# Performance work log

Measured on AMD Instinct MI355X. Metric: run time of the kernel, lower is better.

## Reference

```python
import jax, jax.numpy as jnp
import numpy as np

ALPHA = 1.0

def setup_inputs() -> dict:
    key = jax.random.key(0)
    X = jax.random.normal(key, (8192, 64), dtype=jnp.float32)
    return {"X": X}

def reference(X) -> jnp.ndarray:
    # Pairwise squared L2 distances via GEMM trick: ||x_i||^2 + ||x_j||^2 - 2 x_i.x_j
    sq = jnp.sum(X * X, axis=1)                      # [N]
    d2 = sq[:, None] + sq[None, :] - 2.0 * (X @ X.T)  # [N, N]
    d2 = jnp.maximum(d2, 0.0)
    # sigma^2 = alpha * mean(d2), detached (no grad through bandwidth)
    sigma_sq = ALPHA * jax.lax.stop_gradient(jnp.mean(d2))
    return jnp.exp(-d2 / (2.0 * sigma_sq))
```

## Files before the change

### kernel.cpp

```cpp
#include <hip/hip_runtime.h>
#include <hip/hip_bf16.h>

#define N 8192
#define D 64

typedef __attribute__((ext_vector_type(8))) short bf16x8;
typedef __attribute__((ext_vector_type(4))) float f32x4;

__device__ inline unsigned short f2b(float f) {
    __hip_bfloat16 h = __float2bfloat16(f);
    return __builtin_bit_cast(unsigned short, h);
}

__global__ __launch_bounds__(256) void gk_prep(const float4* __restrict__ X4,
                                               ushort4* __restrict__ Xb4,
                                               float* __restrict__ sq) {
    const int g = blockIdx.x * 256 + threadIdx.x;
    float4 v = X4[g];
    ushort4 b;
    b.x = f2b(v.x); b.y = f2b(v.y); b.z = f2b(v.z); b.w = f2b(v.w);
    Xb4[g] = b;
    float ss = v.x * v.x + v.y * v.y + v.z * v.z + v.w * v.w;
    ss += __shfl_xor(ss, 8, 16);
    ss += __shfl_xor(ss, 4, 16);
    ss += __shfl_xor(ss, 2, 16);
    ss += __shfl_xor(ss, 1, 16);
    if ((threadIdx.x & 15) == 0) sq[g >> 4] = ss;
}

__global__ __launch_bounds__(256) void gk_colsum(const float* __restrict__ X,
                                                 float* __restrict__ V) {
    __shared__ float red[256];
    const int c = blockIdx.x;
    float s = 0.f;
    for (int r = threadIdx.x; r < N; r += 256) s += X[r * D + c];
    red[threadIdx.x] = s;
    __syncthreads();
    for (int off = 128; off > 0; off >>= 1) {
        if (threadIdx.x < off) red[threadIdx.x] += red[threadIdx.x + off];
        __syncthreads();
    }
    if (threadIdx.x == 0) V[c] = red[0];
}

__global__ __launch_bounds__(256) void gk_finalize(const float* __restrict__ sq,
                                                   const float* __restrict__ V,
                                                   float* __restrict__ scal) {
    __shared__ float red[256];
    float s = 0.f;
    for (int r = threadIdx.x; r < N; r += 256) s += sq[r];
    red[threadIdx.x] = s;
    __syncthreads();
    for (int off = 128; off > 0; off >>= 1) {
        if (threadIdx.x < off) red[threadIdx.x] += red[threadIdx.x + off];
        __syncthreads();
    }
    const float S = red[0];
    __syncthreads();
    float v = (threadIdx.x < D) ? V[threadIdx.x] : 0.f;
    red[threadIdx.x] = v * v;
    __syncthreads();
    for (int off = 128; off > 0; off >>= 1) {
        if (threadIdx.x < off) red[threadIdx.x] += red[threadIdx.x + off];
        __syncthreads();
    }
    if (threadIdx.x == 0) {
        const float Vsq = red[0];
        const float fN = (float)N;
        const float mean = 2.f * S / fN - 2.f * Vsq / (fN * fN);
        const float sigma_sq = 1.0f * mean;
        scal[0] = 1.f / (2.f * sigma_sq);
    }
}

__global__ __launch_bounds__(256) void gk_main(const unsigned short* __restrict__ Xb,
                                               const float* __restrict__ sq,
                                               const float* __restrict__ scal,
                                               float* __restrict__ out) {
    const int lane = threadIdx.x & 63;
    const int wave = threadIdx.x >> 6;
    const int i0 = blockIdx.x * 64 + wave * 16;
    const int j0 = blockIdx.y * 128;
    const int m = lane & 15;
    const int q = lane >> 4;
    const float c0 = scal[0];

    const bf16x8* Arow = reinterpret_cast<const bf16x8*>(Xb + (i0 + m) * D + 8 * q);
    const bf16x8 a0 = Arow[0];
    const bf16x8 a1 = Arow[4];

    f32x4 acc[8];
#pragma unroll
    for (int t = 0; t < 8; ++t) acc[t] = (f32x4){0.f, 0.f, 0.f, 0.f};

#pragma unroll
    for (int t = 0; t < 8; ++t) {
        const bf16x8* Brow =
            reinterpret_cast<const bf16x8*>(Xb + (j0 + t * 16 + m) * D + 8 * q);
        const bf16x8 b0 = Brow[0];
        const bf16x8 b1 = Brow[4];
        acc[t] = __builtin_amdgcn_mfma_f32_16x16x32_bf16(a0, b0, acc[t], 0, 0, 0);
        acc[t] = __builtin_amdgcn_mfma_f32_16x16x32_bf16(a1, b1, acc[t], 0, 0, 0);
    }

    float sqi[4];
#pragma unroll
    for (int r = 0; r < 4; ++r) sqi[r] = sq[i0 + 4 * q + r];

#pragma unroll
    for (int t = 0; t < 8; ++t) {
        const int col = j0 + t * 16 + m;
        const float sqj = sq[col];
#pragma unroll
        for (int r = 0; r < 4; ++r) {
            float d2 = sqi[r] + sqj - 2.0f * acc[t][r];
            d2 = fmaxf(d2, 0.0f);
            out[(size_t)(i0 + 4 * q + r) * N + col] = __expf(-d2 * c0);
        }
    }
}

extern "C" void kernel_launch(void* const* d_in, const int* in_sizes, int n_in,
                              void* d_out, int out_size, void* d_ws, size_t ws_size,
                              hipStream_t stream) {
    const float* X = (const float*)d_in[0];
    float* out = (float*)d_out;

    char* ws = (char*)d_ws;
    unsigned short* Xb = (unsigned short*)ws;
    float* sq = (float*)(ws + 1048576);
    float* V  = (float*)(ws + 1048576 + 32768);
    float* scal = (float*)(ws + 1048576 + 32768 + 256);

    gk_prep<<<512, 256, 0, stream>>>((const float4*)X, (ushort4*)Xb, sq);
    gk_colsum<<<D, 256, 0, stream>>>(X, V);
    gk_finalize<<<1, 256, 0, stream>>>(sq, V, scal);

    dim3 grid(N / 64, N / 128);
    gk_main<<<grid, 256, 0, stream>>>(Xb, sq, scal, out);
}
```

Measured before the change: 314.6 us.

## Fuse column sums into prep and write the symmetric output transposed with float4 stores

The column-sum kernel is removed. Per-block partial column sums are now computed in the prep kernel with wave shuffles and shared memory, and the finalize kernel reduces them. This drops one launch and the strided column reads. The main kernel uses the symmetry of the kernel matrix to write each lane's four accumulator rows as a single float4 into the transposed position, replacing four scalar stores per tile. It also hoists the sq[j] loads next to the MFMA loop and uses an fma for the distance. The transposed write is only correct because the output is symmetric, and the workspace layout grows for the partial sums.

```diff
diff --git a/kernel.cpp b/kernel.cpp
--- a/kernel.cpp
+++ b/kernel.cpp
@@ -14,62 +14,74 @@
 
 __global__ __launch_bounds__(256) void gk_prep(const float4* __restrict__ X4,
                                                ushort4* __restrict__ Xb4,
-                                               float* __restrict__ sq) {
-    const int g = blockIdx.x * 256 + threadIdx.x;
+                                               float* __restrict__ sq,
+                                               float* __restrict__ Vp) {
+    __shared__ float cs[4][64];
+    const int tid = threadIdx.x;
+    const int g = blockIdx.x * 256 + tid;
     float4 v = X4[g];
     ushort4 b;
     b.x = f2b(v.x); b.y = f2b(v.y); b.z = f2b(v.z); b.w = f2b(v.w);
     Xb4[g] = b;
+
     float ss = v.x * v.x + v.y * v.y + v.z * v.z + v.w * v.w;
     ss += __shfl_xor(ss, 8, 16);
     ss += __shfl_xor(ss, 4, 16);
     ss += __shfl_xor(ss, 2, 16);
     ss += __shfl_xor(ss, 1, 16);
-    if ((threadIdx.x & 15) == 0) sq[g >> 4] = ss;
-}
+    if ((tid & 15) == 0) sq[g >> 4] = ss;
 
-__global__ __launch_bounds__(256) void gk_colsum(const float* __restrict__ X,
-                                                 float* __restrict__ V) {
-    __shared__ float red[256];
-    const int c = blockIdx.x;
-    float s = 0.f;
-    for (int r = threadIdx.x; r < N; r += 256) s += X[r * D + c];
-    red[threadIdx.x] = s;
+    float4 cv = v;
+    cv.x += __shfl_xor(cv.x, 16); cv.x += __shfl_xor(cv.x, 32);
+    cv.y += __shfl_xor(cv.y, 16); cv.y += __shfl_xor(cv.y, 32);
+    cv.z += __shfl_xor(cv.z, 16); cv.z += __shfl_xor(cv.z, 32);
+    cv.w += __shfl_xor(cv.w, 16); cv.w += __shfl_xor(cv.w, 32);
+    const int wave = tid >> 6;
+    const int lane = tid & 63;
+    if (lane < 16) *(float4*)&cs[wave][lane * 4] = cv;
     __syncthreads();
-    for (int off = 128; off > 0; off >>= 1) {
-        if (threadIdx.x < off) red[threadIdx.x] += red[threadIdx.x + off];
-        __syncthreads();
-    }
-    if (threadIdx.x == 0) V[c] = red[0];
+    if (tid < 64) Vp[blockIdx.x * 64 + tid] = cs[0][tid] + cs[1][tid] + cs[2][tid] + cs[3][tid];
 }
 
 __global__ __launch_bounds__(256) void gk_finalize(const float* __restrict__ sq,
-                                                   const float* __restrict__ V,
+                                                   const float* __restrict__ Vp,
                                                    float* __restrict__ scal) {
     __shared__ float red[256];
+    const int tid = threadIdx.x;
+
     float s = 0.f;
-    for (int r = threadIdx.x; r < N; r += 256) s += sq[r];
-    red[threadIdx.x] = s;
+    for (int r = tid; r < N; r += 256) s += sq[r];
+    red[tid] = s;
     __syncthreads();
     for (int off = 128; off > 0; off >>= 1) {
-        if (threadIdx.x < off) red[threadIdx.x] += red[threadIdx.x + off];
+        if (tid < off) red[tid] += red[tid + off];
         __syncthreads();
     }
     const float S = red[0];
     __syncthreads();
-    float v = (threadIdx.x < D) ? V[threadIdx.x] : 0.f;
-    red[threadIdx.x] = v * v;
+
+    const int c = tid & 63, k = tid >> 6;
+    float v = 0.f;
+    for (int bb = k; bb < 512; bb += 4) v += Vp[bb * 64 + c];
+    red[tid] = v;
+    __syncthreads();
+    float vsq_part = 0.f;
+    if (tid < 64) {
+        const float vc = red[tid] + red[tid + 64] + red[tid + 128] + red[tid + 192];
+        vsq_part = vc * vc;
+    }
+    __syncthreads();
+    red[tid] = vsq_part;
     __syncthreads();
     for (int off = 128; off > 0; off >>= 1) {
-        if (threadIdx.x < off) red[threadIdx.x] += red[threadIdx.x + off];
+        if (tid < off) red[tid] += red[tid + off];
         __syncthreads();
     }
-    if (threadIdx.x == 0) {
+    if (tid == 0) {
         const float Vsq = red[0];
         const float fN = (float)N;
         const float mean = 2.f * S / fN - 2.f * Vsq / (fN * fN);
-        const float sigma_sq = 1.0f * mean;
-        scal[0] = 1.f / (2.f * sigma_sq);
+        scal[0] = 1.f / (2.f * mean);
     }
 }
 
@@ -90,6 +102,7 @@
     const bf16x8 a1 = Arow[4];
 
     f32x4 acc[8];
+    float sqj[8];
 #pragma unroll
     for (int t = 0; t < 8; ++t) acc[t] = (f32x4){0.f, 0.f, 0.f, 0.f};
 
@@ -99,6 +112,7 @@
             reinterpret_cast<const bf16x8*>(Xb + (j0 + t * 16 + m) * D + 8 * q);
         const bf16x8 b0 = Brow[0];
         const bf16x8 b1 = Brow[4];
+        sqj[t] = sq[j0 + t * 16 + m];
         acc[t] = __builtin_amdgcn_mfma_f32_16x16x32_bf16(a0, b0, acc[t], 0, 0, 0);
         acc[t] = __builtin_amdgcn_mfma_f32_16x16x32_bf16(a1, b1, acc[t], 0, 0, 0);
     }
@@ -109,14 +123,16 @@
 
 #pragma unroll
     for (int t = 0; t < 8; ++t) {
-        const int col = j0 + t * 16 + m;
-        const float sqj = sq[col];
+        const int row = j0 + t * 16 + m;
+        const float sj = sqj[t];
+        float4 o;
 #pragma unroll
         for (int r = 0; r < 4; ++r) {
-            float d2 = sqi[r] + sqj - 2.0f * acc[t][r];
+            float d2 = __builtin_fmaf(acc[t][r], -2.0f, sqi[r] + sj);
             d2 = fmaxf(d2, 0.0f);
-            out[(size_t)(i0 + 4 * q + r) * N + col] = __expf(-d2 * c0);
+            (&o.x)[r] = __expf(-d2 * c0);
         }
+        *(float4*)&out[(size_t)row * N + i0 + 4 * q] = o;
     }
 }
 
@@ -128,13 +144,12 @@
 
     char* ws = (char*)d_ws;
     unsigned short* Xb = (unsigned short*)ws;
-    float* sq = (float*)(ws + 1048576);
-    float* V  = (float*)(ws + 1048576 + 32768);
-    float* scal = (float*)(ws + 1048576 + 32768 + 256);
+    float* sq   = (float*)(ws + 1048576);
+    float* Vp   = (float*)(ws + 1048576 + 32768);
+    float* scal = (float*)(ws + 1048576 + 32768 + 131072);
 
-    gk_prep<<<512, 256, 0, stream>>>((const float4*)X, (ushort4*)Xb, sq);
-    gk_colsum<<<D, 256, 0, stream>>>(X, V);
-    gk_finalize<<<1, 256, 0, stream>>>(sq, V, scal);
+    gk_prep<<<512, 256, 0, stream>>>((const float4*)X, (ushort4*)Xb, sq, Vp);
+    gk_finalize<<<1, 256, 0, stream>>>(sq, Vp, scal);
 
     dim3 grid(N / 64, N / 128);
     gk_main<<<grid, 256, 0, stream>>>(Xb, sq, scal, out);
```

Result: slower. 343.8 us (+9.3%).
